# Kernel tuning notes

Hardware: AMD Instinct MI355X
Metric: run time of the kernel (lower is better)

The kernel has to match this reference:

```python
import jax, jax.numpy as jnp
import numpy as np

B, S, H, F, E = 2, 2048, 1024, 4096, 8  # batch, seq, hidden, ffn, num_experts


def setup_inputs() -> dict:
    key = jax.random.key(0)
    ks = jax.random.split(key, 4)
    x = jax.random.normal(ks[0], (B, S, H), dtype=jnp.float32)
    w_router = jax.random.normal(ks[1], (H, E), dtype=jnp.float32) * 0.02
    w1 = jax.random.normal(ks[2], (E, H, F), dtype=jnp.float32) * 0.02
    b1 = jnp.zeros((E, F), dtype=jnp.float32)
    w2 = jax.random.normal(ks[3], (E, F, H), dtype=jnp.float32) * 0.02
    b2 = jnp.zeros((E, H), dtype=jnp.float32)
    return {"x": x, "w_router": w_router, "w1": w1, "b1": b1, "w2": w2, "b2": b2}


def reference(x, w_router, w1, b1, w2, b2):
    """Top-1 MoE layer: route -> per-expert FFN -> weighted combine.

    Faithful to ExpertParallelWrapper._process_moe_layer on a single group:
    router picks one expert per token with a routing weight; tokens are
    dispatched to experts (here expressed as a static mask over the fixed
    expert set), processed by the expert FFN, and scatter-combined back
    weighted by the routing probability.
    """
    Bs, Ss, Hs = x.shape
    n_experts = w1.shape[0]
    # Router: per-token logits -> softmax -> top-1 expert + weight
    logits = jnp.einsum('bsh,he->bse', x, w_router)          # [B,S,E]
    probs = jax.nn.softmax(logits, axis=-1)
    sel = jnp.argmax(probs, axis=-1)                          # [B,S] selected expert
    wgt = jnp.take_along_axis(probs, sel[..., None], axis=-1)[..., 0]  # [B,S]

    xt = x.reshape(-1, Hs)        # [T,H] flat tokens
    sel_t = sel.reshape(-1)       # [T]
    wgt_t = wgt.reshape(-1)       # [T]

    out = jnp.zeros_like(xt)
    # Static loop over the small fixed expert set (dispatch/combine via mask).
    for e in range(n_experts):
        h = jax.nn.relu(xt @ w1[e] + b1[e])   # [T,F]
        y = h @ w2[e] + b2[e]                 # [T,H]
        m = (sel_t == e).astype(xt.dtype) * wgt_t
        out = out + m[:, None] * y
    return out.reshape(Bs, Ss, Hs)
```

## Files before the change

### kernel.cpp

```cpp
#include <hip/hip_runtime.h>
#include <math.h>

#define T_TOK 4096
#define H_DIM 1024
#define F_DIM 4096
#define E_NUM 8
#define BK 64
#define KSPLIT 4

typedef __attribute__((ext_vector_type(8))) short bhalf8_t;
typedef __attribute__((ext_vector_type(8))) unsigned short ushort8_t;
typedef __attribute__((ext_vector_type(4))) float f32x4_t;

__device__ __forceinline__ unsigned short f2bf(float f) {
  unsigned int u = __float_as_uint(f);
  return (unsigned short)((u + 0x7fffu + ((u >> 16) & 1u)) >> 16);
}

__device__ __forceinline__ void gload16(const void* g, void* l) {
  __builtin_amdgcn_global_load_lds(
      (const __attribute__((address_space(1))) unsigned int*)g,
      (__attribute__((address_space(3))) unsigned int*)l, 16, 0, 0);
}

__global__ void k_init(int* counts) {
  if (threadIdx.x < E_NUM) counts[threadIdx.x] = 0;
}

__global__ __launch_bounds__(256) void k_router(const float* __restrict__ x,
                                                const float* __restrict__ wr,
                                                int* __restrict__ sel, float* __restrict__ wgt,
                                                int* __restrict__ counts) {
  const int t = blockIdx.x * 4 + (threadIdx.x >> 6);
  const int lane = threadIdx.x & 63;
  const float* xr = x + (size_t)t * H_DIM;
  double acc[E_NUM] = {0, 0, 0, 0, 0, 0, 0, 0};
  for (int h = lane; h < H_DIM; h += 64) {
    const double xv = (double)xr[h];
    const float* w = wr + (size_t)h * E_NUM;
#pragma unroll
    for (int e = 0; e < E_NUM; ++e) acc[e] += xv * (double)w[e];
  }
#pragma unroll
  for (int e = 0; e < E_NUM; ++e) {
#pragma unroll
    for (int off = 32; off > 0; off >>= 1) acc[e] += __shfl_down(acc[e], off, 64);
  }
  if (lane == 0) {
    double m = acc[0];
    int a = 0;
#pragma unroll
    for (int e = 1; e < E_NUM; ++e)
      if (acc[e] > m) { m = acc[e]; a = e; }
    double s = 0.0;
#pragma unroll
    for (int e = 0; e < E_NUM; ++e) s += exp(acc[e] - m);
    sel[t] = a;
    wgt[t] = (float)(1.0 / s);
    atomicAdd(&counts[a], 1);
  }
}

__global__ void k_prefix(const int* __restrict__ counts, int* __restrict__ offs,
                         int* __restrict__ cursors) {
  if (threadIdx.x == 0 && blockIdx.x == 0) {
    int s = 0;
    for (int e = 0; e < E_NUM; ++e) {
      offs[e] = s;
      cursors[e] = s;
      s += counts[e];
    }
    offs[E_NUM] = s;
  }
}

__global__ void k_scatter(const float* __restrict__ x, const int* __restrict__ sel,
                          const float* __restrict__ wgt, int* __restrict__ cursors,
                          int* __restrict__ s2t, float* __restrict__ wgtS,
                          int* __restrict__ eS, unsigned short* __restrict__ Xs) {
  const int t = blockIdx.x;
  __shared__ int sslot;
  if (threadIdx.x == 0) {
    const int e = sel[t];
    const int slot = atomicAdd(&cursors[e], 1);
    sslot = slot;
    s2t[slot] = t;
    wgtS[slot] = wgt[t];
    eS[slot] = e;
  }
  __syncthreads();
  const int slot = sslot;
  const float4 v = reinterpret_cast<const float4*>(x + (size_t)t * H_DIM)[threadIdx.x];
  ushort4 o;
  o.x = f2bf(v.x); o.y = f2bf(v.y); o.z = f2bf(v.z); o.w = f2bf(v.w);
  reinterpret_cast<ushort4*>(Xs + (size_t)slot * H_DIM)[threadIdx.x] = o;
}

__global__ __launch_bounds__(256) void k_transpose(const float* __restrict__ in,
                                                   unsigned short* __restrict__ out,
                                                   int K, int N) {
  const int e = blockIdx.z;
  const int n0 = blockIdx.x * 64;
  const int k0 = blockIdx.y * 64;
  __shared__ float tile[64][65];
  const float* src = in + (size_t)e * K * N;
  unsigned short* dst = out + (size_t)e * N * K;
  const int l = threadIdx.x;
  const int lr = l >> 4;
  const int lc = (l & 15) * 4;
#pragma unroll
  for (int i = 0; i < 64; i += 16) {
    const float4 v = *reinterpret_cast<const float4*>(&src[(size_t)(k0 + lr + i) * N + n0 + lc]);
    tile[lr + i][lc] = v.x;
    tile[lr + i][lc + 1] = v.y;
    tile[lr + i][lc + 2] = v.z;
    tile[lr + i][lc + 3] = v.w;
  }
  __syncthreads();
  const int kk = (l & 7) * 8;
  const int nr = l >> 3;
#pragma unroll
  for (int i = 0; i < 64; i += 32) {
    const int n = nr + i;
    ushort8_t o;
#pragma unroll
    for (int j = 0; j < 8; ++j) o[j] = f2bf(tile[kk + j][n]);
    *reinterpret_cast<ushort8_t*>(&dst[(size_t)(n0 + n) * K + k0 + kk]) = o;
  }
}

__global__ __launch_bounds__(256, 4) void k_ffn1(const unsigned short* __restrict__ Xs,
                                                 const unsigned short* __restrict__ Wt,
                                                 const float* __restrict__ b1,
                                                 unsigned short* __restrict__ Hws,
                                                 const int* __restrict__ offs) {
  const int e = blockIdx.z;
  const int off = offs[e];
  const int cnt = offs[e + 1] - off;
  const int m0 = blockIdx.y * 128;
  if (m0 >= cnt) return;
  const int n0 = blockIdx.x * 64;
  const int msize = cnt - m0;

  __shared__ short lA[128 * BK];
  __shared__ short lB[64 * BK];

  const int tid = threadIdx.x;
  const int lane = tid & 63;
  const int wv = tid >> 6;
  const int wm = (wv >> 1) * 64;
  const int wn = (wv & 1) * 32;

  const int sRow = lane >> 3;
  const int cc = lane & 7;
  const int gch = cc ^ sRow;

  const unsigned short* Abase = Xs + (size_t)off * H_DIM;
  const unsigned short* Bbase = Wt + (size_t)e * F_DIM * H_DIM + (size_t)n0 * H_DIM;

  f32x4_t acc[4][2];
#pragma unroll
  for (int i = 0; i < 4; ++i)
#pragma unroll
    for (int j = 0; j < 2; ++j) acc[i][j] = (f32x4_t){0.f, 0.f, 0.f, 0.f};

  const int q = lane >> 4;
  const int r16 = lane & 15;
  const int sw = r16 & 7;

  for (int k0 = 0; k0 < H_DIM; k0 += BK) {
    __syncthreads();
#pragma unroll
    for (int i = 0; i < 4; ++i) {
      const int g = wv * 4 + i;
      const int row = g * 8 + sRow;
      const int ar = (row < msize) ? row : 0;
      gload16(Abase + (size_t)(m0 + ar) * H_DIM + k0 + gch * 8, &lA[g * 8 * BK]);
    }
#pragma unroll
    for (int i = 0; i < 2; ++i) {
      const int g = wv * 2 + i;
      const int row = g * 8 + sRow;
      gload16(Bbase + (size_t)row * H_DIM + k0 + gch * 8, &lB[g * 8 * BK]);
    }
    __syncthreads();

#pragma unroll
    for (int step = 0; step < 2; ++step) {
      const int slot = (step * 4 + q) ^ sw;
      bhalf8_t af[4], bf[2];
#pragma unroll
      for (int mi = 0; mi < 4; ++mi)
        af[mi] = *reinterpret_cast<const bhalf8_t*>(&lA[(wm + mi * 16 + r16) * BK + slot * 8]);
#pragma unroll
      for (int ni = 0; ni < 2; ++ni)
        bf[ni] = *reinterpret_cast<const bhalf8_t*>(&lB[(wn + ni * 16 + r16) * BK + slot * 8]);
#pragma unroll
      for (int mi = 0; mi < 4; ++mi)
#pragma unroll
        for (int ni = 0; ni < 2; ++ni)
          acc[mi][ni] = __builtin_amdgcn_mfma_f32_16x16x32_bf16(af[mi], bf[ni], acc[mi][ni], 0, 0, 0);
    }
  }

  const int c = lane & 15;
#pragma unroll
  for (int ni = 0; ni < 2; ++ni) {
    const int col = n0 + wn + ni * 16 + c;
    const float bias = b1[e * F_DIM + col];
#pragma unroll
    for (int mi = 0; mi < 4; ++mi) {
      const int rbase = wm + mi * 16 + q * 4;
#pragma unroll
      for (int r = 0; r < 4; ++r) {
        const int row = rbase + r;
        if (row < msize) {
          float v = acc[mi][ni][r] + bias;
          v = fmaxf(v, 0.0f);
          Hws[(size_t)(off + m0 + row) * F_DIM + col] = f2bf(v);
        }
      }
    }
  }
}

__global__ __launch_bounds__(256, 4) void k_ffn2_sk(const unsigned short* __restrict__ Hws,
                                                    const unsigned short* __restrict__ Wt,
                                                    const int* __restrict__ offs,
                                                    float* __restrict__ P) {
  const int e = blockIdx.z >> 2;
  const int ks = blockIdx.z & 3;
  const int off = offs[e];
  const int cnt = offs[e + 1] - off;
  const int m0 = blockIdx.y * 128;
  if (m0 >= cnt) return;
  const int n0 = blockIdx.x * 128;
  const int msize = cnt - m0;
  const int kbeg = ks * (F_DIM / KSPLIT);
  const int kend = kbeg + (F_DIM / KSPLIT);

  __shared__ short lA[128 * BK];
  __shared__ short lB[128 * BK];

  const int tid = threadIdx.x;
  const int lane = tid & 63;
  const int wv = tid >> 6;
  const int wm = (wv >> 1) * 64;
  const int wn = (wv & 1) * 64;

  const int sRow = lane >> 3;
  const int cc = lane & 7;
  const int gch = cc ^ sRow;

  const unsigned short* Abase = Hws + (size_t)off * F_DIM;
  const unsigned short* Bbase = Wt + (size_t)e * H_DIM * F_DIM + (size_t)n0 * F_DIM;

  f32x4_t acc[4][4];
#pragma unroll
  for (int i = 0; i < 4; ++i)
#pragma unroll
    for (int j = 0; j < 4; ++j) acc[i][j] = (f32x4_t){0.f, 0.f, 0.f, 0.f};

  const int q = lane >> 4;
  const int r16 = lane & 15;
  const int sw = r16 & 7;

  for (int k0 = kbeg; k0 < kend; k0 += BK) {
    __syncthreads();
#pragma unroll
    for (int i = 0; i < 4; ++i) {
      const int g = wv * 4 + i;
      const int row = g * 8 + sRow;
      const int ar = (row < msize) ? row : 0;
      gload16(Abase + (size_t)(m0 + ar) * F_DIM + k0 + gch * 8, &lA[g * 8 * BK]);
      gload16(Bbase + (size_t)row * F_DIM + k0 + gch * 8, &lB[g * 8 * BK]);
    }
    __syncthreads();

#pragma unroll
    for (int step = 0; step < 2; ++step) {
      const int slot = (step * 4 + q) ^ sw;
      bhalf8_t af[4], bf[4];
#pragma unroll
      for (int mi = 0; mi < 4; ++mi)
        af[mi] = *reinterpret_cast<const bhalf8_t*>(&lA[(wm + mi * 16 + r16) * BK + slot * 8]);
#pragma unroll
      for (int ni = 0; ni < 4; ++ni)
        bf[ni] = *reinterpret_cast<const bhalf8_t*>(&lB[(wn + ni * 16 + r16) * BK + slot * 8]);
#pragma unroll
      for (int mi = 0; mi < 4; ++mi)
#pragma unroll
        for (int ni = 0; ni < 4; ++ni)
          acc[mi][ni] = __builtin_amdgcn_mfma_f32_16x16x32_bf16(af[mi], bf[ni], acc[mi][ni], 0, 0, 0);
    }
  }

  const int c = lane & 15;
  float* Pb = P + (size_t)ks * T_TOK * H_DIM;
#pragma unroll
  for (int mi = 0; mi < 4; ++mi) {
    const int rbase = wm + mi * 16 + q * 4;
#pragma unroll
    for (int r = 0; r < 4; ++r) {
      const int row = rbase + r;
      if (row >= msize) continue;
      float* prow = Pb + (size_t)(off + m0 + row) * H_DIM;
#pragma unroll
      for (int ni = 0; ni < 4; ++ni) prow[n0 + wn + ni * 16 + c] = acc[mi][ni][r];
    }
  }
}

__global__ __launch_bounds__(256) void k_reduce(const float* __restrict__ P,
                                                const float* __restrict__ b2,
                                                const int* __restrict__ s2t,
                                                const int* __restrict__ eS,
                                                const float* __restrict__ wgtS,
                                                float* __restrict__ out) {
  const int srow = blockIdx.x;
  const int tok = s2t[srow];
  const int e = eS[srow];
  const float w = wgtS[srow];
  const int i = threadIdx.x;
  const size_t rowoff = (size_t)srow * H_DIM / 4 + i;
  const float4 p0 = reinterpret_cast<const float4*>(P)[rowoff];
  const float4 p1 = reinterpret_cast<const float4*>(P + (size_t)T_TOK * H_DIM)[rowoff];
  const float4 p2 = reinterpret_cast<const float4*>(P + (size_t)2 * T_TOK * H_DIM)[rowoff];
  const float4 p3 = reinterpret_cast<const float4*>(P + (size_t)3 * T_TOK * H_DIM)[rowoff];
  const float4 b = reinterpret_cast<const float4*>(b2 + (size_t)e * H_DIM)[i];
  float4 o;
  o.x = w * (p0.x + p1.x + p2.x + p3.x + b.x);
  o.y = w * (p0.y + p1.y + p2.y + p3.y + b.y);
  o.z = w * (p0.z + p1.z + p2.z + p3.z + b.z);
  o.w = w * (p0.w + p1.w + p2.w + p3.w + b.w);
  reinterpret_cast<float4*>(out + (size_t)tok * H_DIM)[i] = o;
}

__global__ __launch_bounds__(256, 4) void k_ffn2_direct(const unsigned short* __restrict__ Hws,
                                                        const unsigned short* __restrict__ Wt,
                                                        const float* __restrict__ b2,
                                                        const int* __restrict__ offs,
                                                        const int* __restrict__ s2t,
                                                        const float* __restrict__ wgtS,
                                                        float* __restrict__ out) {
  const int e = blockIdx.z;
  const int off = offs[e];
  const int cnt = offs[e + 1] - off;
  const int m0 = blockIdx.y * 128;
  if (m0 >= cnt) return;
  const int n0 = blockIdx.x * 128;
  const int msize = cnt - m0;

  __shared__ short lA[128 * BK];
  __shared__ short lB[128 * BK];

  const int tid = threadIdx.x;
  const int lane = tid & 63;
  const int wv = tid >> 6;
  const int wm = (wv >> 1) * 64;
  const int wn = (wv & 1) * 64;

  const int sRow = lane >> 3;
  const int cc = lane & 7;
  const int gch = cc ^ sRow;

  const unsigned short* Abase = Hws + (size_t)off * F_DIM;
  const unsigned short* Bbase = Wt + (size_t)e * H_DIM * F_DIM + (size_t)n0 * F_DIM;

  f32x4_t acc[4][4];
#pragma unroll
  for (int i = 0; i < 4; ++i)
#pragma unroll
    for (int j = 0; j < 4; ++j) acc[i][j] = (f32x4_t){0.f, 0.f, 0.f, 0.f};

  const int q = lane >> 4;
  const int r16 = lane & 15;
  const int sw = r16 & 7;

  for (int k0 = 0; k0 < F_DIM; k0 += BK) {
    __syncthreads();
#pragma unroll
    for (int i = 0; i < 4; ++i) {
      const int g = wv * 4 + i;
      const int row = g * 8 + sRow;
      const int ar = (row < msize) ? row : 0;
      gload16(Abase + (size_t)(m0 + ar) * F_DIM + k0 + gch * 8, &lA[g * 8 * BK]);
      gload16(Bbase + (size_t)row * F_DIM + k0 + gch * 8, &lB[g * 8 * BK]);
    }
    __syncthreads();

#pragma unroll
    for (int step = 0; step < 2; ++step) {
      const int slot = (step * 4 + q) ^ sw;
      bhalf8_t af[4], bf[4];
#pragma unroll
      for (int mi = 0; mi < 4; ++mi)
        af[mi] = *reinterpret_cast<const bhalf8_t*>(&lA[(wm + mi * 16 + r16) * BK + slot * 8]);
#pragma unroll
      for (int ni = 0; ni < 4; ++ni)
        bf[ni] = *reinterpret_cast<const bhalf8_t*>(&lB[(wn + ni * 16 + r16) * BK + slot * 8]);
#pragma unroll
      for (int mi = 0; mi < 4; ++mi)
#pragma unroll
        for (int ni = 0; ni < 4; ++ni)
          acc[mi][ni] = __builtin_amdgcn_mfma_f32_16x16x32_bf16(af[mi], bf[ni], acc[mi][ni], 0, 0, 0);
    }
  }

  const int c = lane & 15;
#pragma unroll
  for (int mi = 0; mi < 4; ++mi) {
    const int rbase = wm + mi * 16 + q * 4;
#pragma unroll
    for (int r = 0; r < 4; ++r) {
      const int row = rbase + r;
      if (row >= msize) continue;
      const int srow = off + m0 + row;
      const int tok = s2t[srow];
      const float w = wgtS[srow];
      float* orow = out + (size_t)tok * H_DIM;
#pragma unroll
      for (int ni = 0; ni < 4; ++ni) {
        const int col = n0 + wn + ni * 16 + c;
        orow[col] = w * (acc[mi][ni][r] + b2[e * H_DIM + col]);
      }
    }
  }
}

extern "C" void kernel_launch(void* const* d_in, const int* in_sizes, int n_in,
                              void* d_out, int out_size, void* d_ws, size_t ws_size,
                              hipStream_t stream) {
  const float* x  = (const float*)d_in[0];
  const float* wr = (const float*)d_in[1];
  const float* w1 = (const float*)d_in[2];
  const float* b1 = (const float*)d_in[3];
  const float* w2 = (const float*)d_in[4];
  const float* b2 = (const float*)d_in[5];
  float* out = (float*)d_out;

  char* ws = (char*)d_ws;
  unsigned short* WT  = (unsigned short*)(ws);
  unsigned short* XS  = (unsigned short*)(ws + 67108864);
  unsigned short* HWS = (unsigned short*)(ws + 67108864 + 8388608);
  char* ctrl = ws + 109051904;
  int*   sel     = (int*)(ctrl);
  int*   s2t     = (int*)(ctrl + 16384);
  float* wgt     = (float*)(ctrl + 32768);
  float* wgtS    = (float*)(ctrl + 49152);
  int*   eS      = (int*)(ctrl + 65536);
  int*   counts  = (int*)(ctrl + 81920);
  int*   offs    = (int*)(ctrl + 81920 + 64);
  int*   cursors = (int*)(ctrl + 81920 + 128);
  float* P = (float*)(ws + 109150208);
  const bool use_splitk = ws_size >= (size_t)(109150208) + (size_t)KSPLIT * T_TOK * H_DIM * 4;

  k_init<<<1, 64, 0, stream>>>(counts);
  k_router<<<T_TOK / 4, 256, 0, stream>>>(x, wr, sel, wgt, counts);
  k_prefix<<<1, 1, 0, stream>>>(counts, offs, cursors);
  k_scatter<<<T_TOK, 256, 0, stream>>>(x, sel, wgt, cursors, s2t, wgtS, eS, XS);

  k_transpose<<<dim3(F_DIM / 64, H_DIM / 64, E_NUM), 256, 0, stream>>>(w1, WT, H_DIM, F_DIM);
  k_ffn1<<<dim3(F_DIM / 64, T_TOK / 128, E_NUM), 256, 0, stream>>>(XS, WT, b1, HWS, offs);

  k_transpose<<<dim3(H_DIM / 64, F_DIM / 64, E_NUM), 256, 0, stream>>>(w2, WT, F_DIM, H_DIM);
  if (use_splitk) {
    k_ffn2_sk<<<dim3(H_DIM / 128, T_TOK / 128, E_NUM * KSPLIT), 256, 0, stream>>>(HWS, WT, offs, P);
    k_reduce<<<T_TOK, 256, 0, stream>>>(P, b2, s2t, eS, wgtS, out);
  } else {
    k_ffn2_direct<<<dim3(H_DIM / 128, T_TOK / 128, E_NUM), 256, 0, stream>>>(HWS, WT, b2, offs, s2t, wgtS, out);
  }
}
```

Before: 551.9 us.

## Fuse weight transposes with router and FFN1 kernels, widen FFN1 tile

Merges the w1 transpose with the router into one launch and runs the w2 transpose inside the FFN1 kernel as extra blocks, so the transposes overlap with compute and fewer kernels are launched. Expert counting moves from global atomics in the router to a shared-memory histogram in the prefix kernel. FFN1 tiles grow from 128x64 to 128x128, which gives more reuse per block but uses more registers. When workspace is large enough, separate buffers for WT1 and WT2 are used and P aliases WT1. Transposing w2 in the same kernel competes with the GEMM blocks for bandwidth and CU slots.

Measured after the change: 500.7 us. 9.3% less time.

```diff
diff --git a/kernel.cpp b/kernel.cpp
--- a/kernel.cpp
+++ b/kernel.cpp
@@ -23,15 +23,51 @@
       (__attribute__((address_space(3))) unsigned int*)l, 16, 0, 0);
 }
 
-__global__ void k_init(int* counts) {
-  if (threadIdx.x < E_NUM) counts[threadIdx.x] = 0;
-}
-
-__global__ __launch_bounds__(256) void k_router(const float* __restrict__ x,
-                                                const float* __restrict__ wr,
-                                                int* __restrict__ sel, float* __restrict__ wgt,
-                                                int* __restrict__ counts) {
-  const int t = blockIdx.x * 4 + (threadIdx.x >> 6);
+__device__ __forceinline__ void transpose_dev(const float* __restrict__ src,
+                                              unsigned short* __restrict__ dst,
+                                              int K, int N, int bx, int by, void* sm_) {
+  float(*tile)[65] = (float(*)[65])sm_;
+  const int n0 = bx * 64;
+  const int k0 = by * 64;
+  const int l = threadIdx.x;
+  const int lr = l >> 4;
+  const int lc = (l & 15) * 4;
+#pragma unroll
+  for (int i = 0; i < 64; i += 16) {
+    const float4 v = *reinterpret_cast<const float4*>(&src[(size_t)(k0 + lr + i) * N + n0 + lc]);
+    tile[lr + i][lc] = v.x;
+    tile[lr + i][lc + 1] = v.y;
+    tile[lr + i][lc + 2] = v.z;
+    tile[lr + i][lc + 3] = v.w;
+  }
+  __syncthreads();
+  const int kk = (l & 7) * 8;
+  const int nr = l >> 3;
+#pragma unroll
+  for (int i = 0; i < 64; i += 32) {
+    const int n = nr + i;
+    ushort8_t o;
+#pragma unroll
+    for (int j = 0; j < 8; ++j) o[j] = f2bf(tile[kk + j][n]);
+    *reinterpret_cast<ushort8_t*>(&dst[(size_t)(n0 + n) * K + k0 + kk]) = o;
+  }
+}
+
+__global__ __launch_bounds__(256) void k_pre(const float* __restrict__ x,
+                                             const float* __restrict__ wr,
+                                             const float* __restrict__ w1,
+                                             unsigned short* __restrict__ WT1,
+                                             int* __restrict__ sel, float* __restrict__ wgt) {
+  __shared__ __align__(16) char sm[64 * 65 * 4];
+  if (blockIdx.x < 64) {
+    transpose_dev(w1 + (size_t)blockIdx.z * H_DIM * F_DIM,
+                  WT1 + (size_t)blockIdx.z * F_DIM * H_DIM,
+                  H_DIM, F_DIM, blockIdx.x, blockIdx.y, sm);
+    return;
+  }
+  if (blockIdx.z != 0) return;
+  const int bid = blockIdx.y * 64 + (blockIdx.x - 64);
+  const int t = bid * 4 + (threadIdx.x >> 6);
   const int lane = threadIdx.x & 63;
   const float* xr = x + (size_t)t * H_DIM;
   double acc[E_NUM] = {0, 0, 0, 0, 0, 0, 0, 0};
@@ -57,18 +93,22 @@
     for (int e = 0; e < E_NUM; ++e) s += exp(acc[e] - m);
     sel[t] = a;
     wgt[t] = (float)(1.0 / s);
-    atomicAdd(&counts[a], 1);
-  }
-}
-
-__global__ void k_prefix(const int* __restrict__ counts, int* __restrict__ offs,
+  }
+}
+
+__global__ void k_prefix(const int* __restrict__ sel, int* __restrict__ offs,
                          int* __restrict__ cursors) {
-  if (threadIdx.x == 0 && blockIdx.x == 0) {
+  __shared__ int h[E_NUM];
+  if (threadIdx.x < E_NUM) h[threadIdx.x] = 0;
+  __syncthreads();
+  for (int i = threadIdx.x; i < T_TOK; i += 256) atomicAdd(&h[sel[i]], 1);
+  __syncthreads();
+  if (threadIdx.x == 0) {
     int s = 0;
     for (int e = 0; e < E_NUM; ++e) {
       offs[e] = s;
       cursors[e] = s;
-      s += counts[e];
+      s += h[e];
     }
     offs[E_NUM] = s;
   }
@@ -96,60 +136,37 @@
   reinterpret_cast<ushort4*>(Xs + (size_t)slot * H_DIM)[threadIdx.x] = o;
 }
 
-__global__ __launch_bounds__(256) void k_transpose(const float* __restrict__ in,
-                                                   unsigned short* __restrict__ out,
-                                                   int K, int N) {
-  const int e = blockIdx.z;
-  const int n0 = blockIdx.x * 64;
-  const int k0 = blockIdx.y * 64;
-  __shared__ float tile[64][65];
-  const float* src = in + (size_t)e * K * N;
-  unsigned short* dst = out + (size_t)e * N * K;
-  const int l = threadIdx.x;
-  const int lr = l >> 4;
-  const int lc = (l & 15) * 4;
-#pragma unroll
-  for (int i = 0; i < 64; i += 16) {
-    const float4 v = *reinterpret_cast<const float4*>(&src[(size_t)(k0 + lr + i) * N + n0 + lc]);
-    tile[lr + i][lc] = v.x;
-    tile[lr + i][lc + 1] = v.y;
-    tile[lr + i][lc + 2] = v.z;
-    tile[lr + i][lc + 3] = v.w;
-  }
-  __syncthreads();
-  const int kk = (l & 7) * 8;
-  const int nr = l >> 3;
-#pragma unroll
-  for (int i = 0; i < 64; i += 32) {
-    const int n = nr + i;
-    ushort8_t o;
-#pragma unroll
-    for (int j = 0; j < 8; ++j) o[j] = f2bf(tile[kk + j][n]);
-    *reinterpret_cast<ushort8_t*>(&dst[(size_t)(n0 + n) * K + k0 + kk]) = o;
-  }
-}
-
-__global__ __launch_bounds__(256, 4) void k_ffn1(const unsigned short* __restrict__ Xs,
-                                                 const unsigned short* __restrict__ Wt,
-                                                 const float* __restrict__ b1,
-                                                 unsigned short* __restrict__ Hws,
-                                                 const int* __restrict__ offs) {
+__global__ __launch_bounds__(256, 4) void k_mid(const unsigned short* __restrict__ Xs,
+                                                const unsigned short* __restrict__ Wt,
+                                                const float* __restrict__ b1,
+                                                unsigned short* __restrict__ Hws,
+                                                const int* __restrict__ offs,
+                                                const float* __restrict__ w2,
+                                                unsigned short* __restrict__ WT2) {
+  __shared__ __align__(16) char sm[32768];
+  if (blockIdx.x >= 32) {
+    const int id = blockIdx.y * 32 + (blockIdx.x - 32);
+    transpose_dev(w2 + (size_t)blockIdx.z * F_DIM * H_DIM,
+                  WT2 + (size_t)blockIdx.z * H_DIM * F_DIM,
+                  F_DIM, H_DIM, id & 15, id >> 4, sm);
+    return;
+  }
   const int e = blockIdx.z;
   const int off = offs[e];
   const int cnt = offs[e + 1] - off;
   const int m0 = blockIdx.y * 128;
   if (m0 >= cnt) return;
-  const int n0 = blockIdx.x * 64;
+  const int n0 = blockIdx.x * 128;
   const int msize = cnt - m0;
 
-  __shared__ short lA[128 * BK];
-  __shared__ short lB[64 * BK];
+  short* lA = (short*)sm;
+  short* lB = (short*)(sm + 16384);
 
   const int tid = threadIdx.x;
   const int lane = tid & 63;
   const int wv = tid >> 6;
   const int wm = (wv >> 1) * 64;
-  const int wn = (wv & 1) * 32;
+  const int wn = (wv & 1) * 64;
 
   const int sRow = lane >> 3;
   const int cc = lane & 7;
@@ -158,11 +175,11 @@
   const unsigned short* Abase = Xs + (size_t)off * H_DIM;
   const unsigned short* Bbase = Wt + (size_t)e * F_DIM * H_DIM + (size_t)n0 * H_DIM;
 
-  f32x4_t acc[4][2];
+  f32x4_t acc[4][4];
 #pragma unroll
   for (int i = 0; i < 4; ++i)
 #pragma unroll
-    for (int j = 0; j < 2; ++j) acc[i][j] = (f32x4_t){0.f, 0.f, 0.f, 0.f};
+    for (int j = 0; j < 4; ++j) acc[i][j] = (f32x4_t){0.f, 0.f, 0.f, 0.f};
 
   const int q = lane >> 4;
   const int r16 = lane & 15;
@@ -176,11 +193,6 @@
       const int row = g * 8 + sRow;
       const int ar = (row < msize) ? row : 0;
       gload16(Abase + (size_t)(m0 + ar) * H_DIM + k0 + gch * 8, &lA[g * 8 * BK]);
-    }
-#pragma unroll
-    for (int i = 0; i < 2; ++i) {
-      const int g = wv * 2 + i;
-      const int row = g * 8 + sRow;
       gload16(Bbase + (size_t)row * H_DIM + k0 + gch * 8, &lB[g * 8 * BK]);
     }
     __syncthreads();
@@ -188,24 +200,24 @@
 #pragma unroll
     for (int step = 0; step < 2; ++step) {
       const int slot = (step * 4 + q) ^ sw;
-      bhalf8_t af[4], bf[2];
+      bhalf8_t af[4], bf[4];
 #pragma unroll
       for (int mi = 0; mi < 4; ++mi)
         af[mi] = *reinterpret_cast<const bhalf8_t*>(&lA[(wm + mi * 16 + r16) * BK + slot * 8]);
 #pragma unroll
-      for (int ni = 0; ni < 2; ++ni)
+      for (int ni = 0; ni < 4; ++ni)
         bf[ni] = *reinterpret_cast<const bhalf8_t*>(&lB[(wn + ni * 16 + r16) * BK + slot * 8]);
 #pragma unroll
       for (int mi = 0; mi < 4; ++mi)
 #pragma unroll
-        for (int ni = 0; ni < 2; ++ni)
+        for (int ni = 0; ni < 4; ++ni)
           acc[mi][ni] = __builtin_amdgcn_mfma_f32_16x16x32_bf16(af[mi], bf[ni], acc[mi][ni], 0, 0, 0);
     }
   }
 
   const int c = lane & 15;
 #pragma unroll
-  for (int ni = 0; ni < 2; ++ni) {
+  for (int ni = 0; ni < 4; ++ni) {
     const int col = n0 + wn + ni * 16 + c;
     const float bias = b1[e * F_DIM + col];
 #pragma unroll
@@ -336,6 +348,14 @@
   reinterpret_cast<float4*>(out + (size_t)tok * H_DIM)[i] = o;
 }
 
+__global__ __launch_bounds__(256) void k_transpose(const float* __restrict__ in,
+                                                   unsigned short* __restrict__ out,
+                                                   int K, int N) {
+  __shared__ __align__(16) char sm[64 * 65 * 4];
+  transpose_dev(in + (size_t)blockIdx.z * K * N, out + (size_t)blockIdx.z * N * K,
+                K, N, blockIdx.x, blockIdx.y, sm);
+}
+
 __global__ __launch_bounds__(256, 4) void k_ffn2_direct(const unsigned short* __restrict__ Hws,
                                                         const unsigned short* __restrict__ Wt,
                                                         const float* __restrict__ b2,
@@ -440,34 +460,46 @@
   float* out = (float*)d_out;
 
   char* ws = (char*)d_ws;
-  unsigned short* WT  = (unsigned short*)(ws);
-  unsigned short* XS  = (unsigned short*)(ws + 67108864);
-  unsigned short* HWS = (unsigned short*)(ws + 67108864 + 8388608);
-  char* ctrl = ws + 109051904;
-  int*   sel     = (int*)(ctrl);
-  int*   s2t     = (int*)(ctrl + 16384);
-  float* wgt     = (float*)(ctrl + 32768);
-  float* wgtS    = (float*)(ctrl + 49152);
-  int*   eS      = (int*)(ctrl + 65536);
-  int*   counts  = (int*)(ctrl + 81920);
-  int*   offs    = (int*)(ctrl + 81920 + 64);
-  int*   cursors = (int*)(ctrl + 81920 + 128);
-  float* P = (float*)(ws + 109150208);
-  const bool use_splitk = ws_size >= (size_t)(109150208) + (size_t)KSPLIT * T_TOK * H_DIM * 4;
-
-  k_init<<<1, 64, 0, stream>>>(counts);
-  k_router<<<T_TOK / 4, 256, 0, stream>>>(x, wr, sel, wgt, counts);
-  k_prefix<<<1, 1, 0, stream>>>(counts, offs, cursors);
-  k_scatter<<<T_TOK, 256, 0, stream>>>(x, sel, wgt, cursors, s2t, wgtS, eS, XS);
-
-  k_transpose<<<dim3(F_DIM / 64, H_DIM / 64, E_NUM), 256, 0, stream>>>(w1, WT, H_DIM, F_DIM);
-  k_ffn1<<<dim3(F_DIM / 64, T_TOK / 128, E_NUM), 256, 0, stream>>>(XS, WT, b1, HWS, offs);
-
-  k_transpose<<<dim3(H_DIM / 64, F_DIM / 64, E_NUM), 256, 0, stream>>>(w2, WT, F_DIM, H_DIM);
-  if (use_splitk) {
-    k_ffn2_sk<<<dim3(H_DIM / 128, T_TOK / 128, E_NUM * KSPLIT), 256, 0, stream>>>(HWS, WT, offs, P);
+  const size_t NEED_FAST = 67108864ull * 2 + 8388608 + 33554432 + 98304;
+  if (ws_size >= NEED_FAST) {
+    unsigned short* WT1 = (unsigned short*)(ws);
+    unsigned short* WT2 = (unsigned short*)(ws + 67108864);
+    unsigned short* XS  = (unsigned short*)(ws + 134217728);
+    unsigned short* HWS = (unsigned short*)(ws + 142606336);
+    char* ctrl = ws + 176160768;
+    int*   sel     = (int*)(ctrl);
+    int*   s2t     = (int*)(ctrl + 16384);
+    float* wgt     = (float*)(ctrl + 32768);
+    float* wgtS    = (float*)(ctrl + 49152);
+    int*   eS      = (int*)(ctrl + 65536);
+    int*   offs    = (int*)(ctrl + 81920);
+    int*   cursors = (int*)(ctrl + 81984);
+    float* P = (float*)ws;
+
+    k_pre<<<dim3(128, 16, 8), 256, 0, stream>>>(x, wr, w1, WT1, sel, wgt);
+    k_prefix<<<1, 256, 0, stream>>>(sel, offs, cursors);
+    k_scatter<<<T_TOK, 256, 0, stream>>>(x, sel, wgt, cursors, s2t, wgtS, eS, XS);
+    k_mid<<<dim3(64, 32, 8), 256, 0, stream>>>(XS, WT1, b1, HWS, offs, w2, WT2);
+    k_ffn2_sk<<<dim3(H_DIM / 128, T_TOK / 128, E_NUM * KSPLIT), 256, 0, stream>>>(HWS, WT2, offs, P);
     k_reduce<<<T_TOK, 256, 0, stream>>>(P, b2, s2t, eS, wgtS, out);
   } else {
+    unsigned short* WT  = (unsigned short*)(ws);
+    unsigned short* XS  = (unsigned short*)(ws + 67108864);
+    unsigned short* HWS = (unsigned short*)(ws + 75497472);
+    char* ctrl = ws + 109051904;
+    int*   sel     = (int*)(ctrl);
+    int*   s2t     = (int*)(ctrl + 16384);
+    float* wgt     = (float*)(ctrl + 32768);
+    float* wgtS    = (float*)(ctrl + 49152);
+    int*   eS      = (int*)(ctrl + 65536);
+    int*   offs    = (int*)(ctrl + 81920);
+    int*   cursors = (int*)(ctrl + 81984);
+
+    k_pre<<<dim3(128, 16, 8), 256, 0, stream>>>(x, wr, w1, WT, sel, wgt);
+    k_prefix<<<1, 256, 0, stream>>>(sel, offs, cursors);
+    k_scatter<<<T_TOK, 256, 0, stream>>>(x, sel, wgt, cursors, s2t, wgtS, eS, XS);
+    k_mid<<<dim3(32, 32, 8), 256, 0, stream>>>(XS, WT, b1, HWS, offs, w2, (unsigned short*)0);
+    k_transpose<<<dim3(H_DIM / 64, F_DIM / 64, E_NUM), 256, 0, stream>>>(w2, WT, F_DIM, H_DIM);
     k_ffn2_direct<<<dim3(H_DIM / 128, T_TOK / 128, E_NUM), 256, 0, stream>>>(HWS, WT, b2, offs, s2t, wgtS, out);
   }
 }
```
